# Kernel optimization log

Measured on AMD Instinct MI355X. Metric: run time of the kernel, lower is better.

## Reference

```python
import jax, jax.numpy as jnp
import numpy as np

H, DH = 12, 64            # num heads, head dim (hidden=768)
ATTN_WINDOW = 512         # Longformer attention_window
W = ATTN_WINDOW // 2      # one-sided window (attend W tokens each side + self)


def setup_inputs() -> dict:
    key = jax.random.key(0)
    ks = jax.random.split(key, 4)
    B, S, D = 2, 4096, 768
    sc = 0.02
    return {
        "hidden_states": jax.random.normal(ks[0], (B, S, D), jnp.float32),
        "attention_mask": jnp.zeros((B, S), jnp.float32),  # 0 = normal local attention
        "Wq": jax.random.normal(ks[1], (D, D), jnp.float32) * sc,
        "bq": jnp.zeros((D,), jnp.float32),
        "Wk": jax.random.normal(ks[2], (D, D), jnp.float32) * sc,
        "bk": jnp.zeros((D,), jnp.float32),
        "Wv": jax.random.normal(ks[3], (D, D), jnp.float32) * sc,
        "bv": jnp.zeros((D,), jnp.float32),
    }


def _windows(x):
    # x: [B, H, nb+2, w, D] overlapping 3-block windows -> [B, H, nb, 3w, D]
    return jnp.concatenate([x[:, :, :-2], x[:, :, 1:-1], x[:, :, 2:]], axis=3)


def reference(hidden_states, attention_mask, Wq, bq, Wk, bk, Wv, bv):
    B, S, D = hidden_states.shape
    w = W
    nb = S // w  # number of query blocks

    # QKV projections; Longformer scales q by 1/sqrt(head_dim)
    q = (hidden_states @ Wq + bq) / jnp.sqrt(jnp.asarray(DH, hidden_states.dtype))
    k = hidden_states @ Wk + bk
    v = hidden_states @ Wv + bv

    def split_heads(x):  # [B,S,D] -> [B,H,S,DH]
        return x.reshape(B, S, H, DH).transpose(0, 2, 1, 3)

    q, k, v = split_heads(q), split_heads(k), split_heads(v)

    qb = q.reshape(B, H, nb, w, DH)
    kp = jnp.pad(k, ((0, 0), (0, 0), (w, w), (0, 0))).reshape(B, H, nb + 2, w, DH)
    vp = jnp.pad(v, ((0, 0), (0, 0), (w, w), (0, 0))).reshape(B, H, nb + 2, w, DH)
    kw, vw = _windows(kp), _windows(vp)  # [B,H,nb,3w,DH]

    # banded scores: each query block attends its 3w key window
    scores = jnp.einsum('bhnqd,bhnkd->bhnqk', qb, kw)  # [B,H,nb,w,3w]

    # sliding-window diagonal mask: |i - j| <= w and key index in [0, S)
    q_idx = (jnp.arange(nb) * w)[:, None] + jnp.arange(w)[None, :]          # [nb,w]
    k_idx = (jnp.arange(nb) * w - w)[:, None] + jnp.arange(3 * w)[None, :]  # [nb,3w]
    rel = k_idx[:, None, :] - q_idx[:, :, None]                              # [nb,w,3w]
    in_win = (jnp.abs(rel) <= w) & (k_idx[:, None, :] >= 0) & (k_idx[:, None, :] < S)

    # key padding mask (attention_mask < 0 => masked token)
    masked = attention_mask < 0  # [B,S]
    kmp = jnp.pad(masked, ((0, 0), (w, w))).reshape(B, nb + 2, w)
    kmw = jnp.concatenate([kmp[:, :-2], kmp[:, 1:-1], kmp[:, 2:]], axis=2)  # [B,nb,3w]

    allowed = in_win[None, None] & ~kmw[:, None, :, None, :]  # [B,H,nb,w,3w]
    scores = jnp.where(allowed, scores, jnp.asarray(-1e9, scores.dtype))

    probs = jax.nn.softmax(scores, axis=-1)
    # zero out attention rows of masked (padding) queries, as Longformer does
    probs = jnp.where(masked.reshape(B, 1, nb, w, 1), jnp.zeros((), probs.dtype), probs)

    out = jnp.einsum('bhnqk,bhnkd->bhnqd', probs, vw)  # [B,H,nb,w,DH]
    out = out.reshape(B, H, S, DH).transpose(0, 2, 1, 3).reshape(B, S, H * DH)
    return out
```

## Files before the change

### kernel.cpp

```cpp
#include <hip/hip_runtime.h>
#include <hip/hip_bf16.h>

#define BATCH 2
#define SEQ   4096
#define DM    768
#define NHEAD 12
#define HDIM  64
#define WIN   256

typedef unsigned short u16;
typedef unsigned int u32;
typedef __attribute__((ext_vector_type(8))) short bf16x8;
typedef __attribute__((ext_vector_type(4))) float f32x4;
typedef __attribute__((ext_vector_type(8))) unsigned short u16x8;
typedef __attribute__((ext_vector_type(4))) unsigned short u16x4;
typedef __attribute__((ext_vector_type(2))) unsigned int u32x2;

__device__ __forceinline__ u16 f2bf(float x) {
    unsigned u = __builtin_bit_cast(unsigned, x);
    return (u16)((u + 0x7FFFu + ((u >> 16) & 1u)) >> 16);
}

#define GLL16(g, l) __builtin_amdgcn_global_load_lds( \
    (const __attribute__((address_space(1))) u32*)(g), \
    (__attribute__((address_space(3))) u32*)(l), 16, 0, 0)

__global__ __launch_bounds__(256) void prep(
    const float* __restrict__ in, u16* __restrict__ Abf,
    const float* __restrict__ Wq, const float* __restrict__ Wk,
    const float* __restrict__ Wv, u16* __restrict__ Wt)
{
    __shared__ float tile[32][33];
    const int bid = blockIdx.x;
    if (bid < 3072) {
        size_t i = ((size_t)bid * 256 + threadIdx.x) * 8;
        float4 a = *(const float4*)(in + i);
        float4 b = *(const float4*)(in + i + 4);
        u16x8 r;
        r[0] = f2bf(a.x); r[1] = f2bf(a.y); r[2] = f2bf(a.z); r[3] = f2bf(a.w);
        r[4] = f2bf(b.x); r[5] = f2bf(b.y); r[6] = f2bf(b.z); r[7] = f2bf(b.w);
        *(u16x8*)(Abf + i) = r;
    } else {
        const int wb = bid - 3072;
        const int mat = wb / 576;
        const int rem = wb - mat * 576;
        const int k0 = (rem / 24) * 32, n0 = (rem % 24) * 32;
        const float* W = (mat == 0) ? Wq : (mat == 1) ? Wk : Wv;
        const int tx = threadIdx.x & 31, ty = threadIdx.x >> 5;
        #pragma unroll
        for (int i = 0; i < 32; i += 8)
            tile[ty + i][tx] = W[(size_t)(k0 + ty + i) * DM + n0 + tx];
        __syncthreads();
        #pragma unroll
        for (int i = 0; i < 32; i += 8)
            Wt[(size_t)mat * DM * DM + (size_t)(n0 + ty + i) * DM + k0 + tx] = f2bf(tile[tx][ty + i]);
    }
}

__global__ __launch_bounds__(256) void qkv_mfma(
    const u16* __restrict__ Abf, const u16* __restrict__ Wt,
    const float* __restrict__ bq, const float* __restrict__ bk, const float* __restrict__ bv,
    u16* __restrict__ qo, u16* __restrict__ ko, u16* __restrict__ vT)
{
    __shared__ u16 lds[2 * 8192];

    const int t  = threadIdx.x;
    const int wv = t >> 6, ln = t & 63, lg = ln >> 4, lm = ln & 15;
    const int wr = wv >> 1, wc = wv & 1;

    const int id  = blockIdx.x + 18 * blockIdx.y;
    const int nid = (id & 7) * 144 + (id >> 3);
    const int bx  = nid % 18, by = nid / 18;

    const int rowStart = by * 128;
    const int nG = bx * 128;
    const int mat = nG / DM;
    const int nColBase = nG - mat * DM;
    const float* bias = (mat == 0) ? bq : (mat == 1) ? bk : bv;
    const u16* Wm = Wt + (size_t)mat * DM * DM;

    f32x4 acc[4][4];
    #pragma unroll
    for (int i = 0; i < 4; i++)
        #pragma unroll
        for (int j = 0; j < 4; j++) acc[i][j] = (f32x4){0.f, 0.f, 0.f, 0.f};

    int r0, c0, r1, c1;
    {
        int byte0 = t * 16;
        int rp = byte0 >> 7, s = (byte0 >> 4) & 7, cf = s ^ (rp & 7);
        r0 = 2 * rp + (cf >> 2); c0 = cf & 3;
        int byte1 = 4096 + t * 16;
        rp = byte1 >> 7; s = (byte1 >> 4) & 7; cf = s ^ (rp & 7);
        r1 = 2 * rp + (cf >> 2); c1 = cf & 3;
    }
    const u16* gA0 = Abf + (size_t)(rowStart + r0) * DM + c0 * 8;
    const u16* gA1 = Abf + (size_t)(rowStart + r1) * DM + c1 * 8;
    const u16* gB0 = Wm  + (size_t)(nColBase + r0) * DM + c0 * 8;
    const u16* gB1 = Wm  + (size_t)(nColBase + r1) * DM + c1 * 8;

    auto STAGE = [&](int buf, int k0) {
        u16* base = lds + buf * 8192 + t * 8;
        GLL16(gA0 + k0, base);
        GLL16(gA1 + k0, base + 2048);
        GLL16(gB0 + k0, base + 4096);
        GLL16(gB1 + k0, base + 6144);
    };

    auto SWO = [&](int row, int lgc) -> int {
        return ((row >> 1) << 6) + (((((row & 1) << 2) + lgc) ^ ((row >> 1) & 7)) << 3);
    };

    auto COMPUTE = [&](int buf) {
        const u16* Ab = lds + buf * 8192;
        const u16* Bb = Ab + 4096;
        bf16x8 af[4], bfr[4];
        #pragma unroll
        for (int mi = 0; mi < 4; mi++) af[mi]  = *(const bf16x8*)(Ab + SWO(wr * 64 + mi * 16 + lm, lg));
        #pragma unroll
        for (int ni = 0; ni < 4; ni++) bfr[ni] = *(const bf16x8*)(Bb + SWO(wc * 64 + ni * 16 + lm, lg));
        __builtin_amdgcn_s_setprio(1);
        #pragma unroll
        for (int mi = 0; mi < 4; mi++)
            #pragma unroll
            for (int ni = 0; ni < 4; ni++)
                acc[mi][ni] = __builtin_amdgcn_mfma_f32_16x16x32_bf16(af[mi], bfr[ni], acc[mi][ni], 0, 0, 0);
        __builtin_amdgcn_s_setprio(0);
    };

    STAGE(0, 0);
    STAGE(1, 32);
    for (int it = 0; it < 23; ++it) {
        asm volatile("s_waitcnt vmcnt(4)" ::: "memory");
        __builtin_amdgcn_s_barrier();
        COMPUTE(it & 1);
        __builtin_amdgcn_s_barrier();
        if (it < 22) STAGE(it & 1, (it + 2) * 32);
    }
    asm volatile("s_waitcnt vmcnt(0)" ::: "memory");
    __builtin_amdgcn_s_barrier();
    COMPUTE(1);

    const int bb = rowStart >> 12;
    const int s0base = (rowStart & 4095) + wr * 64;
    const int col0 = nColBase + wc * 64;
    #pragma unroll
    for (int ni = 0; ni < 4; ni++) {
        const int col = col0 + ni * 16 + lm;
        const int h = col >> 6, d = col & 63;
        const float bsv = bias[col];
        #pragma unroll
        for (int mi = 0; mi < 4; mi++) {
            const int srow = s0base + mi * 16 + lg * 4;
            if (mat == 2) {
                u16x4 pk;
                #pragma unroll
                for (int r = 0; r < 4; r++) pk[r] = f2bf(acc[mi][ni][r] + bsv);
                *(u16x4*)(vT + ((size_t)((bb * NHEAD + h) * HDIM + d)) * SEQ + srow) = pk;
            } else {
                u16* dst = (mat == 0) ? qo : ko;
                const float scl = (mat == 0) ? 0.18033688011112042f : 1.f;
                #pragma unroll
                for (int r = 0; r < 4; r++)
                    dst[((size_t)(bb * NHEAD + h) * SEQ + srow + r) * HDIM + d] =
                        f2bf((acc[mi][ni][r] + bsv) * scl);
            }
        }
    }
}

__global__ __launch_bounds__(256, 4) void attn_mfma(
    const u16* __restrict__ Q, const u16* __restrict__ K,
    const u16* __restrict__ vT, const float* __restrict__ amask,
    float* __restrict__ out)
{
    __shared__ u16 Ks[2][64][64];
    __shared__ u16 Vs[2][64][64];
    __shared__ u16 Pl[4][16][64];

    const int t  = threadIdx.x;
    const int wv = t >> 6, ln = t & 63, lg = ln >> 4, lm = ln & 15;
    const int lm7 = lm & 7;

    const int id  = blockIdx.x + 64 * (blockIdx.y + 12 * blockIdx.z);
    const int nid = (id & 7) * 192 + (id >> 3);
    const int qtile = nid & 63;
    const int hb = nid >> 6;
    const int h = hb % NHEAD, b = hb / NHEAD;

    const int qb0 = qtile * 64;
    const size_t bh = (size_t)(b * NHEAD + h);
    const size_t bS = (size_t)b * SEQ;

    const int qrow = qb0 + wv * 16 + lm;
    const bf16x8 qa0 = *(const bf16x8*)(Q + (bh * SEQ + qrow) * HDIM + lg * 8);
    const bf16x8 qa1 = *(const bf16x8*)(Q + (bh * SEQ + qrow) * HDIM + 32 + lg * 8);

    f32x4 po[4];
    #pragma unroll
    for (int i = 0; i < 4; i++) po[i] = (f32x4){0.f, 0.f, 0.f, 0.f};
    float mrun = -1e9f, lrun = 0.f;

    const int tlo = (4 - qtile) > 0 ? (4 - qtile) : 0;
    const int thi_raw = (SEQ + 192 - qb0) >> 6;
    const int thi = thi_raw < 8 ? thi_raw : 8;

    u16x8 kreg[2], vreg[2];

    auto load_regs = [&](int tt) {
        const int jt0 = qb0 - WIN + tt * 64;
        #pragma unroll
        for (int i = 0; i < 2; i++) {
            int cid = t + i * 256;
            int row = cid >> 3, c = cid & 7;
            kreg[i] = *(const u16x8*)(K  + (bh * SEQ + jt0 + row) * HDIM + c * 8);
            vreg[i] = *(const u16x8*)(vT + (bh * HDIM + row) * SEQ + jt0 + c * 8);
        }
    };
    auto write_lds = [&](int buf) {
        #pragma unroll
        for (int i = 0; i < 2; i++) {
            int cid = t + i * 256;
            int row = cid >> 3, c = cid & 7;
            *(u16x8*)&Ks[buf][row][(c ^ (row & 7)) * 8] = kreg[i];
            *(u16x8*)&Vs[buf][row][(c ^ (row & 7)) * 8] = vreg[i];
        }
    };

    load_regs(tlo);
    write_lds(0);
    __syncthreads();
    int cur = 0;

    for (int tt = tlo; tt <= thi; ++tt) {
        const int jt0 = qb0 - WIN + tt * 64;
        const float kmv = amask[bS + jt0 + ln];
        if (tt < thi) load_regs(tt + 1);

        f32x4 sv[4];
        #pragma unroll
        for (int jf = 0; jf < 4; jf++) sv[jf] = (f32x4){0.f, 0.f, 0.f, 0.f};
        __builtin_amdgcn_s_setprio(1);
        #pragma unroll
        for (int jf = 0; jf < 4; jf++) {
            const u16* kr = &Ks[cur][jf * 16 + lm][0];
            bf16x8 kb0 = *(const bf16x8*)(kr + ((lg ^ lm7) << 3));
            bf16x8 kb1 = *(const bf16x8*)(kr + (((4 + lg) ^ lm7) << 3));
            sv[jf] = __builtin_amdgcn_mfma_f32_16x16x32_bf16(kb0, qa0, sv[jf], 0, 0, 0);
            sv[jf] = __builtin_amdgcn_mfma_f32_16x16x32_bf16(kb1, qa1, sv[jf], 0, 0, 0);
        }
        __builtin_amdgcn_s_setprio(0);

        const bool anym = (__ballot(kmv < 0.f) != 0ULL);
        const bool fastp = (tt >= 1) && (tt <= 7) && !anym;
        if (!fastp) {
            #pragma unroll
            for (int jf = 0; jf < 4; jf++)
                #pragma unroll
                for (int r = 0; r < 4; r++) {
                    const int j = jt0 + jf * 16 + lg * 4 + r;
                    const float km = __shfl(kmv, jf * 16 + lg * 4 + r);
                    const int rel = j - qrow;
                    const bool ok = (rel <= WIN) && (rel >= -WIN) && (km >= 0.f);
                    sv[jf][r] = ok ? sv[jf][r] : -1e9f;
                }
        }

        f32x4 mv = sv[0];
        #pragma unroll
        for (int jf = 1; jf < 4; jf++) {
            mv[0] = fmaxf(mv[0], sv[jf][0]); mv[1] = fmaxf(mv[1], sv[jf][1]);
            mv[2] = fmaxf(mv[2], sv[jf][2]); mv[3] = fmaxf(mv[3], sv[jf][3]);
        }
        float mx = fmaxf(fmaxf(mv[0], mv[1]), fmaxf(mv[2], mv[3]));
        mx = fmaxf(mx, __shfl_xor(mx, 16));
        mx = fmaxf(mx, __shfl_xor(mx, 32));
        const float mnew = fmaxf(mrun, mx);
        const float f = exp2f(mrun - mnew);
        mrun = mnew;

        float p[4][4];
        if (fastp) {
            #pragma unroll
            for (int jf = 0; jf < 4; jf++)
                #pragma unroll
                for (int r = 0; r < 4; r++) p[jf][r] = exp2f(sv[jf][r] - mnew);
        } else {
            #pragma unroll
            for (int jf = 0; jf < 4; jf++)
                #pragma unroll
                for (int r = 0; r < 4; r++)
                    p[jf][r] = sv[jf][r] > -1e8f ? exp2f(sv[jf][r] - mnew) : 0.f;
        }

        float ps = 0.f;
        #pragma unroll
        for (int jf = 0; jf < 4; jf++)
            ps += (p[jf][0] + p[jf][1]) + (p[jf][2] + p[jf][3]);
        ps += __shfl_xor(ps, 16);
        ps += __shfl_xor(ps, 32);
        lrun = lrun * f + ps;

        u32* prow = (u32*)&Pl[wv][lm][0];
        #pragma unroll
        for (int jf = 0; jf < 4; jf++) {
            u32 lo, hi;
            asm("v_cvt_pk_bf16_f32 %0, %1, %2" : "=v"(lo) : "v"(p[jf][0]), "v"(p[jf][1]));
            asm("v_cvt_pk_bf16_f32 %0, %1, %2" : "=v"(hi) : "v"(p[jf][2]), "v"(p[jf][3]));
            const int c = 2 * jf + (lg >> 1);
            u32x2 val; val[0] = lo; val[1] = hi;
            *(u32x2*)(prow + ((c ^ lm7) << 2) + ((lg & 1) << 1)) = val;
        }
        asm volatile("" ::: "memory");

        po[0] *= f; po[1] *= f; po[2] *= f; po[3] *= f;

        const u16* pw = &Pl[wv][lm][0];
        const bf16x8 pa0 = *(const bf16x8*)(pw + ((lg ^ lm7) << 3));
        const bf16x8 pa1 = *(const bf16x8*)(pw + (((4 + lg) ^ lm7) << 3));
        __builtin_amdgcn_s_setprio(1);
        #pragma unroll
        for (int df = 0; df < 4; df++) {
            const u16* vr = &Vs[cur][df * 16 + lm][0];
            bf16x8 va0 = *(const bf16x8*)(vr + ((lg ^ lm7) << 3));
            bf16x8 va1 = *(const bf16x8*)(vr + (((4 + lg) ^ lm7) << 3));
            po[df] = __builtin_amdgcn_mfma_f32_16x16x32_bf16(va0, pa0, po[df], 0, 0, 0);
            po[df] = __builtin_amdgcn_mfma_f32_16x16x32_bf16(va1, pa1, po[df], 0, 0, 0);
        }
        __builtin_amdgcn_s_setprio(0);

        if (tt < thi) write_lds(cur ^ 1);
        __syncthreads();
        cur ^= 1;
    }

    const float qm = amask[bS + qrow];
    const float inv = (lrun > 0.f && qm >= 0.f) ? 1.f / lrun : 0.f;
    float* op = out + (bS + qrow) * DM + h * HDIM;
    #pragma unroll
    for (int df = 0; df < 4; df++) {
        f32x4 o = po[df] * inv;
        *(f32x4*)(op + df * 16 + lg * 4) = o;
    }
}

extern "C" void kernel_launch(void* const* d_in, const int* in_sizes, int n_in,
                              void* d_out, int out_size, void* d_ws, size_t ws_size,
                              hipStream_t stream) {
    const float* hs    = (const float*)d_in[0];
    const float* amask = (const float*)d_in[1];
    const float* Wq    = (const float*)d_in[2];
    const float* bq    = (const float*)d_in[3];
    const float* Wk    = (const float*)d_in[4];
    const float* bk    = (const float*)d_in[5];
    const float* Wv    = (const float*)d_in[6];
    const float* bv    = (const float*)d_in[7];

    const size_t nA   = (size_t)BATCH * SEQ * DM;
    const size_t nW   = (size_t)3 * DM * DM;
    const size_t nQKV = (size_t)BATCH * NHEAD * SEQ * HDIM;

    u16* Abf = (u16*)d_ws;
    u16* Wt  = Abf + nA;
    u16* qb  = Wt + nW;
    u16* kb  = qb + nQKV;
    u16* vT  = kb + nQKV;

    prep<<<4800, 256, 0, stream>>>(hs, Abf, Wq, Wk, Wv, Wt);
    qkv_mfma<<<dim3(3 * DM / 128, BATCH * SEQ / 128), 256, 0, stream>>>(
        Abf, Wt, bq, bk, bv, qb, kb, vT);
    attn_mfma<<<dim3(SEQ / 64, NHEAD, BATCH), 256, 0, stream>>>(
        qb, kb, vT, amask, (float*)d_out);
}
```

Baseline: 93.94 us.

## Process two 64-row query tiles per attention block to reuse K/V tiles

Each attention workgroup now handles 128 query rows (two 64-row halves per wave) instead of 64, iterating over 10 key tiles instead of 9. Each K/V tile staged in LDS is reused by both halves, cutting global K/V traffic and the number of barriers per query row. In exchange it doubles accumulator and score register usage, drops the occupancy hint from launch bounds, and halves the grid to 768 blocks, which may reduce parallelism. The QKV launch dims are rewritten as literals that equal the previous values.

```diff
diff --git a/kernel.cpp b/kernel.cpp
--- a/kernel.cpp
+++ b/kernel.cpp
@@ -169,7 +169,7 @@
     }
 }
 
-__global__ __launch_bounds__(256, 4) void attn_mfma(
+__global__ __launch_bounds__(256) void attn_mfma(
     const u16* __restrict__ Q, const u16* __restrict__ K,
     const u16* __restrict__ vT, const float* __restrict__ amask,
     float* __restrict__ out)
@@ -182,28 +182,32 @@
     const int wv = t >> 6, ln = t & 63, lg = ln >> 4, lm = ln & 15;
     const int lm7 = lm & 7;
 
-    const int id  = blockIdx.x + 64 * (blockIdx.y + 12 * blockIdx.z);
-    const int nid = (id & 7) * 192 + (id >> 3);
-    const int qtile = nid & 63;
-    const int hb = nid >> 6;
+    const int id  = blockIdx.x + 32 * (blockIdx.y + 12 * blockIdx.z);
+    const int nid = (id & 7) * 96 + (id >> 3);
+    const int qtile = nid & 31;
+    const int hb = nid >> 5;
     const int h = hb % NHEAD, b = hb / NHEAD;
 
-    const int qb0 = qtile * 64;
+    const int qb0 = qtile * 128;
     const size_t bh = (size_t)(b * NHEAD + h);
     const size_t bS = (size_t)b * SEQ;
 
-    const int qrow = qb0 + wv * 16 + lm;
-    const bf16x8 qa0 = *(const bf16x8*)(Q + (bh * SEQ + qrow) * HDIM + lg * 8);
-    const bf16x8 qa1 = *(const bf16x8*)(Q + (bh * SEQ + qrow) * HDIM + 32 + lg * 8);
-
-    f32x4 po[4];
+    const int qrow0 = qb0 + wv * 16 + lm;
+    const int qrow1 = qrow0 + 64;
+    const bf16x8 qa00 = *(const bf16x8*)(Q + (bh * SEQ + qrow0) * HDIM + lg * 8);
+    const bf16x8 qa01 = *(const bf16x8*)(Q + (bh * SEQ + qrow0) * HDIM + 32 + lg * 8);
+    const bf16x8 qa10 = *(const bf16x8*)(Q + (bh * SEQ + qrow1) * HDIM + lg * 8);
+    const bf16x8 qa11 = *(const bf16x8*)(Q + (bh * SEQ + qrow1) * HDIM + 32 + lg * 8);
+
+    f32x4 po0[4], po1[4];
     #pragma unroll
-    for (int i = 0; i < 4; i++) po[i] = (f32x4){0.f, 0.f, 0.f, 0.f};
-    float mrun = -1e9f, lrun = 0.f;
-
-    const int tlo = (4 - qtile) > 0 ? (4 - qtile) : 0;
+    for (int i = 0; i < 4; i++) { po0[i] = (f32x4){0.f,0.f,0.f,0.f}; po1[i] = (f32x4){0.f,0.f,0.f,0.f}; }
+    float mrun0 = -1e9f, lrun0 = 0.f, mrun1 = -1e9f, lrun1 = 0.f;
+
+    const int tlo_raw = 4 - (qb0 >> 6);
+    const int tlo = tlo_raw > 0 ? tlo_raw : 0;
     const int thi_raw = (SEQ + 192 - qb0) >> 6;
-    const int thi = thi_raw < 8 ? thi_raw : 8;
+    const int thi = thi_raw < 9 ? thi_raw : 9;
 
     u16x8 kreg[2], vreg[2];
 
@@ -237,110 +241,133 @@
         const float kmv = amask[bS + jt0 + ln];
         if (tt < thi) load_regs(tt + 1);
 
-        f32x4 sv[4];
-        #pragma unroll
-        for (int jf = 0; jf < 4; jf++) sv[jf] = (f32x4){0.f, 0.f, 0.f, 0.f};
+        f32x4 sv0[4], sv1[4];
+        #pragma unroll
+        for (int jf = 0; jf < 4; jf++) { sv0[jf] = (f32x4){0.f,0.f,0.f,0.f}; sv1[jf] = (f32x4){0.f,0.f,0.f,0.f}; }
         __builtin_amdgcn_s_setprio(1);
         #pragma unroll
         for (int jf = 0; jf < 4; jf++) {
             const u16* kr = &Ks[cur][jf * 16 + lm][0];
             bf16x8 kb0 = *(const bf16x8*)(kr + ((lg ^ lm7) << 3));
             bf16x8 kb1 = *(const bf16x8*)(kr + (((4 + lg) ^ lm7) << 3));
-            sv[jf] = __builtin_amdgcn_mfma_f32_16x16x32_bf16(kb0, qa0, sv[jf], 0, 0, 0);
-            sv[jf] = __builtin_amdgcn_mfma_f32_16x16x32_bf16(kb1, qa1, sv[jf], 0, 0, 0);
+            sv0[jf] = __builtin_amdgcn_mfma_f32_16x16x32_bf16(kb0, qa00, sv0[jf], 0, 0, 0);
+            sv0[jf] = __builtin_amdgcn_mfma_f32_16x16x32_bf16(kb1, qa01, sv0[jf], 0, 0, 0);
+            sv1[jf] = __builtin_amdgcn_mfma_f32_16x16x32_bf16(kb0, qa10, sv1[jf], 0, 0, 0);
+            sv1[jf] = __builtin_amdgcn_mfma_f32_16x16x32_bf16(kb1, qa11, sv1[jf], 0, 0, 0);
         }
         __builtin_amdgcn_s_setprio(0);
 
         const bool anym = (__ballot(kmv < 0.f) != 0ULL);
-        const bool fastp = (tt >= 1) && (tt <= 7) && !anym;
-        if (!fastp) {
+
+        auto half = [&](f32x4* sv, f32x4* po, float& mrun, float& lrun,
+                        int qrow, bool fastp) {
+            if (!fastp) {
+                #pragma unroll
+                for (int jf = 0; jf < 4; jf++)
+                    #pragma unroll
+                    for (int r = 0; r < 4; r++) {
+                        const int j = jt0 + jf * 16 + lg * 4 + r;
+                        const float km = __shfl(kmv, jf * 16 + lg * 4 + r);
+                        const int rel = j - qrow;
+                        const bool ok = (rel <= WIN) && (rel >= -WIN) && (km >= 0.f);
+                        sv[jf][r] = ok ? sv[jf][r] : -1e9f;
+                    }
+            }
+
+            f32x4 mv = sv[0];
+            #pragma unroll
+            for (int jf = 1; jf < 4; jf++) {
+                mv[0] = fmaxf(mv[0], sv[jf][0]); mv[1] = fmaxf(mv[1], sv[jf][1]);
+                mv[2] = fmaxf(mv[2], sv[jf][2]); mv[3] = fmaxf(mv[3], sv[jf][3]);
+            }
+            float mx = fmaxf(fmaxf(mv[0], mv[1]), fmaxf(mv[2], mv[3]));
+            mx = fmaxf(mx, __shfl_xor(mx, 16));
+            mx = fmaxf(mx, __shfl_xor(mx, 32));
+            const float mnew = fmaxf(mrun, mx);
+            const float f = exp2f(mrun - mnew);
+            mrun = mnew;
+
+            float p[4][4];
+            if (fastp) {
+                #pragma unroll
+                for (int jf = 0; jf < 4; jf++)
+                    #pragma unroll
+                    for (int r = 0; r < 4; r++) p[jf][r] = exp2f(sv[jf][r] - mnew);
+            } else {
+                #pragma unroll
+                for (int jf = 0; jf < 4; jf++)
+                    #pragma unroll
+                    for (int r = 0; r < 4; r++)
+                        p[jf][r] = sv[jf][r] > -1e8f ? exp2f(sv[jf][r] - mnew) : 0.f;
+            }
+
+            float ps = 0.f;
             #pragma unroll
             for (int jf = 0; jf < 4; jf++)
-                #pragma unroll
-                for (int r = 0; r < 4; r++) {
-                    const int j = jt0 + jf * 16 + lg * 4 + r;
-                    const float km = __shfl(kmv, jf * 16 + lg * 4 + r);
-                    const int rel = j - qrow;
-                    const bool ok = (rel <= WIN) && (rel >= -WIN) && (km >= 0.f);
-                    sv[jf][r] = ok ? sv[jf][r] : -1e9f;
-                }
-        }
-
-        f32x4 mv = sv[0];
-        #pragma unroll
-        for (int jf = 1; jf < 4; jf++) {
-            mv[0] = fmaxf(mv[0], sv[jf][0]); mv[1] = fmaxf(mv[1], sv[jf][1]);
-            mv[2] = fmaxf(mv[2], sv[jf][2]); mv[3] = fmaxf(mv[3], sv[jf][3]);
-        }
-        float mx = fmaxf(fmaxf(mv[0], mv[1]), fmaxf(mv[2], mv[3]));
-        mx = fmaxf(mx, __shfl_xor(mx, 16));
-        mx = fmaxf(mx, __shfl_xor(mx, 32));
-        const float mnew = fmaxf(mrun, mx);
-        const float f = exp2f(mrun - mnew);
-        mrun = mnew;
-
-        float p[4][4];
-        if (fastp) {
+                ps += (p[jf][0] + p[jf][1]) + (p[jf][2] + p[jf][3]);
+            ps += __shfl_xor(ps, 16);
+            ps += __shfl_xor(ps, 32);
+            lrun = lrun * f + ps;
+
+            u32* prow = (u32*)&Pl[wv][lm][0];
             #pragma unroll
-            for (int jf = 0; jf < 4; jf++)
-                #pragma unroll
-                for (int r = 0; r < 4; r++) p[jf][r] = exp2f(sv[jf][r] - mnew);
-        } else {
+            for (int jf = 0; jf < 4; jf++) {
+                u32 lo, hi;
+                asm("v_cvt_pk_bf16_f32 %0, %1, %2" : "=v"(lo) : "v"(p[jf][0]), "v"(p[jf][1]));
+                asm("v_cvt_pk_bf16_f32 %0, %1, %2" : "=v"(hi) : "v"(p[jf][2]), "v"(p[jf][3]));
+                const int c = 2 * jf + (lg >> 1);
+                u32x2 val; val[0] = lo; val[1] = hi;
+                *(u32x2*)(prow + ((c ^ lm7) << 2) + ((lg & 1) << 1)) = val;
+            }
+            asm volatile("" ::: "memory");
+
+            po[0] *= f; po[1] *= f; po[2] *= f; po[3] *= f;
+
+            const u16* pw = &Pl[wv][lm][0];
+            const bf16x8 pa0 = *(const bf16x8*)(pw + ((lg ^ lm7) << 3));
+            const bf16x8 pa1 = *(const bf16x8*)(pw + (((4 + lg) ^ lm7) << 3));
+            __builtin_amdgcn_s_setprio(1);
             #pragma unroll
-            for (int jf = 0; jf < 4; jf++)
-                #pragma unroll
-                for (int r = 0; r < 4; r++)
-                    p[jf][r] = sv[jf][r] > -1e8f ? exp2f(sv[jf][r] - mnew) : 0.f;
-        }
-
-        float ps = 0.f;
-        #pragma unroll
-        for (int jf = 0; jf < 4; jf++)
-            ps += (p[jf][0] + p[jf][1]) + (p[jf][2] + p[jf][3]);
-        ps += __shfl_xor(ps, 16);
-        ps += __shfl_xor(ps, 32);
-        lrun = lrun * f + ps;
-
-        u32* prow = (u32*)&Pl[wv][lm][0];
-        #pragma unroll
-        for (int jf = 0; jf < 4; jf++) {
-            u32 lo, hi;
-            asm("v_cvt_pk_bf16_f32 %0, %1, %2" : "=v"(lo) : "v"(p[jf][0]), "v"(p[jf][1]));
-            asm("v_cvt_pk_bf16_f32 %0, %1, %2" : "=v"(hi) : "v"(p[jf][2]), "v"(p[jf][3]));
-            const int c = 2 * jf + (lg >> 1);
-            u32x2 val; val[0] = lo; val[1] = hi;
-            *(u32x2*)(prow + ((c ^ lm7) << 2) + ((lg & 1) << 1)) = val;
-        }
-        asm volatile("" ::: "memory");
-
-        po[0] *= f; po[1] *= f; po[2] *= f; po[3] *= f;
-
-        const u16* pw = &Pl[wv][lm][0];
-        const bf16x8 pa0 = *(const bf16x8*)(pw + ((lg ^ lm7) << 3));
-        const bf16x8 pa1 = *(const bf16x8*)(pw + (((4 + lg) ^ lm7) << 3));
-        __builtin_amdgcn_s_setprio(1);
-        #pragma unroll
-        for (int df = 0; df < 4; df++) {
-            const u16* vr = &Vs[cur][df * 16 + lm][0];
-            bf16x8 va0 = *(const bf16x8*)(vr + ((lg ^ lm7) << 3));
-            bf16x8 va1 = *(const bf16x8*)(vr + (((4 + lg) ^ lm7) << 3));
-            po[df] = __builtin_amdgcn_mfma_f32_16x16x32_bf16(va0, pa0, po[df], 0, 0, 0);
-            po[df] = __builtin_amdgcn_mfma_f32_16x16x32_bf16(va1, pa1, po[df], 0, 0, 0);
-        }
-        __builtin_amdgcn_s_setprio(0);
+            for (int df = 0; df < 4; df++) {
+                const u16* vr = &Vs[cur][df * 16 + lm][0];
+                bf16x8 va0 = *(const bf16x8*)(vr + ((lg ^ lm7) << 3));
+                bf16x8 va1 = *(const bf16x8*)(vr + (((4 + lg) ^ lm7) << 3));
+                po[df] = __builtin_amdgcn_mfma_f32_16x16x32_bf16(va0, pa0, po[df], 0, 0, 0);
+                po[df] = __builtin_amdgcn_mfma_f32_16x16x32_bf16(va1, pa1, po[df], 0, 0, 0);
+            }
+            __builtin_amdgcn_s_setprio(0);
+            asm volatile("" ::: "memory");
+        };
+
+        const bool fast0 = (tt >= 1) && (tt <= 7) && !anym;
+        const bool fast1 = (tt >= 2) && (tt <= 8) && !anym;
+        half(sv0, po0, mrun0, lrun0, qrow0, fast0);
+        half(sv1, po1, mrun1, lrun1, qrow1, fast1);
 
         if (tt < thi) write_lds(cur ^ 1);
         __syncthreads();
         cur ^= 1;
     }
 
-    const float qm = amask[bS + qrow];
-    const float inv = (lrun > 0.f && qm >= 0.f) ? 1.f / lrun : 0.f;
-    float* op = out + (bS + qrow) * DM + h * HDIM;
-    #pragma unroll
-    for (int df = 0; df < 4; df++) {
-        f32x4 o = po[df] * inv;
-        *(f32x4*)(op + df * 16 + lg * 4) = o;
+    {
+        const float qm = amask[bS + qrow0];
+        const float inv = (lrun0 > 0.f && qm >= 0.f) ? 1.f / lrun0 : 0.f;
+        float* op = out + (bS + qrow0) * DM + h * HDIM;
+        #pragma unroll
+        for (int df = 0; df < 4; df++) {
+            f32x4 o = po0[df] * inv;
+            *(f32x4*)(op + df * 16 + lg * 4) = o;
+        }
+    }
+    {
+        const float qm = amask[bS + qrow1];
+        const float inv = (lrun1 > 0.f && qm >= 0.f) ? 1.f / lrun1 : 0.f;
+        float* op = out + (bS + qrow1) * DM + h * HDIM;
+        #pragma unroll
+        for (int df = 0; df < 4; df++) {
+            f32x4 o = po1[df] * inv;
+            *(f32x4*)(op + df * 16 + lg * 4) = o;
+        }
     }
 }
 
@@ -367,8 +394,8 @@
     u16* vT  = kb + nQKV;
 
     prep<<<4800, 256, 0, stream>>>(hs, Abf, Wq, Wk, Wv, Wt);
-    qkv_mfma<<<dim3(3 * DM / 128, BATCH * SEQ / 128), 256, 0, stream>>>(
+    qkv_mfma<<<dim3(18, 64), 256, 0, stream>>>(
         Abf, Wt, bq, bk, bv, qb, kb, vT);
-    attn_mfma<<<dim3(SEQ / 64, NHEAD, BATCH), 256, 0, stream>>>(
+    attn_mfma<<<dim3(SEQ / 128, NHEAD, BATCH), 256, 0, stream>>>(
         qb, kb, vT, amask, (float*)d_out);
 }
```

After: 116.6 us. +24.2%, slower.

## Fuse fp32-to-bf16 activation conversion into QKV GEMM LDS load path

Applied to the files above, without the earlier changes.

Removes the separate conversion pass that wrote a bf16 copy of hidden_states. The QKV GEMM now streams fp32 activations straight into LDS and converts them to bf16 with packed conversion instructions while building MFMA fragments. This saves one full read and write of the activation tensor plus part of the prep launch. In exchange the GEMM moves twice the A bytes per k-step, uses larger LDS buffers with a new swizzle, and adds conversion ALU work in the inner loop.

```diff
diff --git a/kernel.cpp b/kernel.cpp
--- a/kernel.cpp
+++ b/kernel.cpp
@@ -15,6 +15,7 @@
 typedef __attribute__((ext_vector_type(8))) unsigned short u16x8;
 typedef __attribute__((ext_vector_type(4))) unsigned short u16x4;
 typedef __attribute__((ext_vector_type(2))) unsigned int u32x2;
+typedef __attribute__((ext_vector_type(4))) unsigned int u32x4;
 
 __device__ __forceinline__ u16 f2bf(float x) {
     unsigned u = __builtin_bit_cast(unsigned, x);
@@ -26,43 +27,31 @@
     (__attribute__((address_space(3))) u32*)(l), 16, 0, 0)
 
 __global__ __launch_bounds__(256) void prep(
-    const float* __restrict__ in, u16* __restrict__ Abf,
     const float* __restrict__ Wq, const float* __restrict__ Wk,
     const float* __restrict__ Wv, u16* __restrict__ Wt)
 {
     __shared__ float tile[32][33];
     const int bid = blockIdx.x;
-    if (bid < 3072) {
-        size_t i = ((size_t)bid * 256 + threadIdx.x) * 8;
-        float4 a = *(const float4*)(in + i);
-        float4 b = *(const float4*)(in + i + 4);
-        u16x8 r;
-        r[0] = f2bf(a.x); r[1] = f2bf(a.y); r[2] = f2bf(a.z); r[3] = f2bf(a.w);
-        r[4] = f2bf(b.x); r[5] = f2bf(b.y); r[6] = f2bf(b.z); r[7] = f2bf(b.w);
-        *(u16x8*)(Abf + i) = r;
-    } else {
-        const int wb = bid - 3072;
-        const int mat = wb / 576;
-        const int rem = wb - mat * 576;
-        const int k0 = (rem / 24) * 32, n0 = (rem % 24) * 32;
-        const float* W = (mat == 0) ? Wq : (mat == 1) ? Wk : Wv;
-        const int tx = threadIdx.x & 31, ty = threadIdx.x >> 5;
-        #pragma unroll
-        for (int i = 0; i < 32; i += 8)
-            tile[ty + i][tx] = W[(size_t)(k0 + ty + i) * DM + n0 + tx];
-        __syncthreads();
-        #pragma unroll
-        for (int i = 0; i < 32; i += 8)
-            Wt[(size_t)mat * DM * DM + (size_t)(n0 + ty + i) * DM + k0 + tx] = f2bf(tile[tx][ty + i]);
-    }
+    const int mat = bid / 576;
+    const int rem = bid - mat * 576;
+    const int k0 = (rem / 24) * 32, n0 = (rem % 24) * 32;
+    const float* W = (mat == 0) ? Wq : (mat == 1) ? Wk : Wv;
+    const int tx = threadIdx.x & 31, ty = threadIdx.x >> 5;
+    #pragma unroll
+    for (int i = 0; i < 32; i += 8)
+        tile[ty + i][tx] = W[(size_t)(k0 + ty + i) * DM + n0 + tx];
+    __syncthreads();
+    #pragma unroll
+    for (int i = 0; i < 32; i += 8)
+        Wt[(size_t)mat * DM * DM + (size_t)(n0 + ty + i) * DM + k0 + tx] = f2bf(tile[tx][ty + i]);
 }
 
 __global__ __launch_bounds__(256) void qkv_mfma(
-    const u16* __restrict__ Abf, const u16* __restrict__ Wt,
+    const float* __restrict__ A, const u16* __restrict__ Wt,
     const float* __restrict__ bq, const float* __restrict__ bk, const float* __restrict__ bv,
     u16* __restrict__ qo, u16* __restrict__ ko, u16* __restrict__ vT)
 {
-    __shared__ u16 lds[2 * 8192];
+    __shared__ u16 lds[2 * 12288];
 
     const int t  = threadIdx.x;
     const int wv = t >> 6, ln = t & 63, lg = ln >> 4, lm = ln & 15;
@@ -85,40 +74,53 @@
         #pragma unroll
         for (int j = 0; j < 4; j++) acc[i][j] = (f32x4){0.f, 0.f, 0.f, 0.f};
 
-    int r0, c0, r1, c1;
-    {
-        int byte0 = t * 16;
-        int rp = byte0 >> 7, s = (byte0 >> 4) & 7, cf = s ^ (rp & 7);
-        r0 = 2 * rp + (cf >> 2); c0 = cf & 3;
-        int byte1 = 4096 + t * 16;
-        rp = byte1 >> 7; s = (byte1 >> 4) & 7; cf = s ^ (rp & 7);
-        r1 = 2 * rp + (cf >> 2); c1 = cf & 3;
-    }
-    const u16* gA0 = Abf + (size_t)(rowStart + r0) * DM + c0 * 8;
-    const u16* gA1 = Abf + (size_t)(rowStart + r1) * DM + c1 * 8;
-    const u16* gB0 = Wm  + (size_t)(nColBase + r0) * DM + c0 * 8;
-    const u16* gB1 = Wm  + (size_t)(nColBase + r1) * DM + c1 * 8;
+    const int rA  = t >> 3;
+    const int chA = (t & 7) ^ (rA & 7);
+    const float* gA0 = A + (size_t)(rowStart +  0 + rA) * DM + chA * 4;
+    const float* gA1 = A + (size_t)(rowStart + 32 + rA) * DM + chA * 4;
+    const float* gA2 = A + (size_t)(rowStart + 64 + rA) * DM + chA * 4;
+    const float* gA3 = A + (size_t)(rowStart + 96 + rA) * DM + chA * 4;
+
+    const int cfB = (t & 7) ^ (rA & 7);
+    const int rB  = 2 * rA + (cfB >> 2);
+    const int cB  = (cfB & 3) * 8;
+    const u16* gB0 = Wm + (size_t)(nColBase +  0 + rB) * DM + cB;
+    const u16* gB1 = Wm + (size_t)(nColBase + 64 + rB) * DM + cB;
 
     auto STAGE = [&](int buf, int k0) {
-        u16* base = lds + buf * 8192 + t * 8;
+        u16* base = lds + buf * 12288 + t * 8;
         GLL16(gA0 + k0, base);
         GLL16(gA1 + k0, base + 2048);
-        GLL16(gB0 + k0, base + 4096);
-        GLL16(gB1 + k0, base + 6144);
-    };
-
-    auto SWO = [&](int row, int lgc) -> int {
+        GLL16(gA2 + k0, base + 4096);
+        GLL16(gA3 + k0, base + 6144);
+        GLL16(gB0 + k0, base + 8192);
+        GLL16(gB1 + k0, base + 10240);
+    };
+
+    auto SWOB = [&](int row, int lgc) -> int {
         return ((row >> 1) << 6) + (((((row & 1) << 2) + lgc) ^ ((row >> 1) & 7)) << 3);
     };
 
     auto COMPUTE = [&](int buf) {
-        const u16* Ab = lds + buf * 8192;
-        const u16* Bb = Ab + 4096;
+        const float* Af = (const float*)(lds + buf * 12288);
+        const u16*  Bb  = lds + buf * 12288 + 8192;
         bf16x8 af[4], bfr[4];
         #pragma unroll
-        for (int mi = 0; mi < 4; mi++) af[mi]  = *(const bf16x8*)(Ab + SWO(wr * 64 + mi * 16 + lm, lg));
-        #pragma unroll
-        for (int ni = 0; ni < 4; ni++) bfr[ni] = *(const bf16x8*)(Bb + SWO(wc * 64 + ni * 16 + lm, lg));
+        for (int mi = 0; mi < 4; mi++) {
+            const int r = wr * 64 + mi * 16 + lm;
+            const float* rowp = Af + r * 32;
+            f32x4 a0 = *(const f32x4*)(rowp + ((( 2 * lg)     ^ (r & 7)) << 2));
+            f32x4 a1 = *(const f32x4*)(rowp + (((2 * lg + 1)  ^ (r & 7)) << 2));
+            u32x4 w;
+            asm("v_cvt_pk_bf16_f32 %0, %1, %2" : "=v"(w[0]) : "v"(a0[0]), "v"(a0[1]));
+            asm("v_cvt_pk_bf16_f32 %0, %1, %2" : "=v"(w[1]) : "v"(a0[2]), "v"(a0[3]));
+            asm("v_cvt_pk_bf16_f32 %0, %1, %2" : "=v"(w[2]) : "v"(a1[0]), "v"(a1[1]));
+            asm("v_cvt_pk_bf16_f32 %0, %1, %2" : "=v"(w[3]) : "v"(a1[2]), "v"(a1[3]));
+            af[mi] = __builtin_bit_cast(bf16x8, w);
+        }
+        #pragma unroll
+        for (int ni = 0; ni < 4; ni++)
+            bfr[ni] = *(const bf16x8*)(Bb + SWOB(wc * 64 + ni * 16 + lm, lg));
         __builtin_amdgcn_s_setprio(1);
         #pragma unroll
         for (int mi = 0; mi < 4; mi++)
@@ -131,7 +133,7 @@
     STAGE(0, 0);
     STAGE(1, 32);
     for (int it = 0; it < 23; ++it) {
-        asm volatile("s_waitcnt vmcnt(4)" ::: "memory");
+        asm volatile("s_waitcnt vmcnt(6)" ::: "memory");
         __builtin_amdgcn_s_barrier();
         COMPUTE(it & 1);
         __builtin_amdgcn_s_barrier();
@@ -356,19 +358,17 @@
     const float* Wv    = (const float*)d_in[6];
     const float* bv    = (const float*)d_in[7];
 
-    const size_t nA   = (size_t)BATCH * SEQ * DM;
     const size_t nW   = (size_t)3 * DM * DM;
     const size_t nQKV = (size_t)BATCH * NHEAD * SEQ * HDIM;
 
-    u16* Abf = (u16*)d_ws;
-    u16* Wt  = Abf + nA;
-    u16* qb  = Wt + nW;
-    u16* kb  = qb + nQKV;
-    u16* vT  = kb + nQKV;
-
-    prep<<<4800, 256, 0, stream>>>(hs, Abf, Wq, Wk, Wv, Wt);
-    qkv_mfma<<<dim3(3 * DM / 128, BATCH * SEQ / 128), 256, 0, stream>>>(
-        Abf, Wt, bq, bk, bv, qb, kb, vT);
+    u16* Wt = (u16*)d_ws;
+    u16* qb = Wt + nW;
+    u16* kb = qb + nQKV;
+    u16* vT = kb + nQKV;
+
+    prep<<<1728, 256, 0, stream>>>(Wq, Wk, Wv, Wt);
+    qkv_mfma<<<dim3(18, 64), 256, 0, stream>>>(
+        hs, Wt, bq, bk, bv, qb, kb, vT);
     attn_mfma<<<dim3(SEQ / 64, NHEAD, BATCH), 256, 0, stream>>>(
         qb, kb, vT, amask, (float*)d_out);
 }
```

New measurement: 98.08 us. +4.4%, slower.
